# Performance work log

Hardware: AMD Instinct MI355X
Metric: run time of the kernel (lower is better)

Reference implementation:

```python
import jax, jax.numpy as jnp
import numpy as np

B, N, NCTX, DIM, H, DH, NMEM = 2, 1024, 2048, 1024, 16, 64, 16


def setup_inputs() -> dict:
    key = jax.random.key(0)
    ks = jax.random.split(key, 24)
    r = lambda i, shape, s=1.0: jax.random.normal(ks[i], shape, dtype=jnp.float32) * s
    w = 0.02  # linear weight scale
    return {
        "x": r(0, (B, N, DIM)),
        "context": r(1, (2, B, NCTX, DIM)),
        "wq1": r(2, (DIM, H * DH), w), "wk1": r(3, (DIM, H * DH), w), "wv1": r(4, (DIM, H * DH), w),
        "wq2": r(5, (DIM, H * DH), w), "wk2": r(6, (DIM, H * DH), w), "wv2": r(7, (DIM, H * DH), w),
        "th_pre1": r(8, (H, H), 0.25), "th_post1": r(9, (H, H), 0.25),
        "th_pre2": r(10, (H, H), 0.25), "th_post2": r(11, (H, H), 0.25),
        "scale1": jnp.full((1, H, 1, 1), -3.0, jnp.float32) + r(12, (1, H, 1, 1), 0.05),
        "scale2": jnp.full((1, H, 1, 1), -3.0, jnp.float32) + r(13, (1, H, 1, 1), 0.05),
        "mem_k1": r(14, (H, NMEM, DH)), "mem_v1": r(15, (H, NMEM, DH)),
        "mem_k2": r(16, (H, NMEM, DH)), "mem_v2": r(17, (H, NMEM, DH)),
        "hs1": jnp.ones((1, H, 1, 1), jnp.float32) + r(18, (1, H, 1, 1), 0.05),
        "hs2": jnp.ones((1, H, 1, 1), jnp.float32) + r(19, (1, H, 1, 1), 0.05),
        "wo1": r(20, (H * DH, DIM), w), "wo2": r(21, (H * DH, DIM), w),
    }


def _l2norm(t):
    # F.normalize: t / max(||t||, eps)
    n = jnp.linalg.norm(t, axis=-1, keepdims=True)
    return t / jnp.maximum(n, 1e-12)


def _split_heads(t, b):
    # [b, n, h*d] -> [b, h, n, d]
    return t.reshape(b, -1, H, DH).transpose(0, 2, 1, 3)


def _attend(x, kv, wq, wk, wv, th_pre, th_post, scale_p, mem_k, mem_v, hs, wo):
    b, n, _ = x.shape
    q = _split_heads(x @ wq, b)    # [b,h,n,d]
    k = _split_heads(kv @ wk, b)   # [b,h,j,d]
    v = _split_heads(kv @ wv, b)
    # memory key/values prepended
    k = jnp.concatenate([jnp.broadcast_to(mem_k[None], (b, H, NMEM, DH)), k], axis=2)
    v = jnp.concatenate([jnp.broadcast_to(mem_v[None], (b, H, NMEM, DH)), v], axis=2)
    # qk-norm with learned per-head temperature: scale = 1 / clamp(exp(p), min=0.01)
    q, k = _l2norm(q), _l2norm(k)
    scale = 1.0 / jnp.maximum(jnp.exp(scale_p), 0.01)
    dots = jnp.einsum('bhid,bhjd->bhij', q, k) * scale
    # talking heads: 1x1 Conv2d over head channel == head-mixing matmul
    dots = jnp.einsum('gh,bhij->bgij', th_pre, dots)
    attn = jax.nn.softmax(dots, axis=-1)
    attn = jnp.einsum('gh,bhij->bgij', th_post, attn)
    out = jnp.einsum('bhij,bhjd->bhid', attn, v) * hs  # head_scale
    out = out.transpose(0, 2, 1, 3).reshape(b, n, H * DH)
    return out @ wo


def reference(x, context, wq1, wk1, wv1, wq2, wk2, wv2,
              th_pre1, th_post1, th_pre2, th_post2,
              scale1, scale2, mem_k1, mem_v1, mem_k2, mem_v2,
              hs1, hs2, wo1, wo2):
    o1 = _attend(x, context[0], wq1, wk1, wv1, th_pre1, th_post1, scale1, mem_k1, mem_v1, hs1, wo1)
    o2 = _attend(x, context[1], wq2, wk2, wv2, th_pre2, th_post2, scale2, mem_k2, mem_v2, hs2, wo2)
    return o1 + o2
```

## Files before the change

### kernel.cpp

```cpp
#include <hip/hip_runtime.h>
#include <hip/hip_bf16.h>

#define Bb    2
#define Nn    1024
#define NCTXc 2048
#define DIMd  1024
#define Hh    16
#define DHd   64
#define NMEM  16
#define Jv    (NMEM + NCTXc)
#define JP    2112
#define HJP   (Hh * JP)
#define L2E   1.44269504088896f
#define LDH   1048

typedef _Float16 f16;
typedef _Float16 half8 __attribute__((ext_vector_type(8)));
typedef _Float16 half4 __attribute__((ext_vector_type(4)));
typedef float    f32x4 __attribute__((ext_vector_type(4)));

__device__ __forceinline__ float bf2f(unsigned short u){
  union { unsigned int i; float f; } v; v.i = ((unsigned)u) << 16; return v.f;
}
__device__ __forceinline__ float fin(float v){
  v = (v == v) ? v : 0.f;
  return fminf(fmaxf(v, -65504.f), 65504.f);
}
__device__ __forceinline__ float ldin(const void* p, long i, int isf32){
  return isf32 ? ((const float*)p)[i] : bf2f(((const unsigned short*)p)[i]);
}
__device__ __forceinline__ half8 h8zero(){
  half8 v;
  #pragma unroll
  for (int j = 0; j < 8; j++) v[j] = (f16)0.f;
  return v;
}

__global__ void detect_dtype(const void* __restrict__ p, int* __restrict__ flag, int n){
  const unsigned short* ub = (const unsigned short*)p;
  const float* fp = (const float*)p;
  int t = threadIdx.x;
  float bb = 0.f, bf = 0.f;
  for (int i = t; i < n; i += 64){
    float vb = bf2f(ub[i]);
    if (!(vb == vb) || fabsf(vb) > 1000.f) bb += 1.f;
    float vf = fp[i];
    if (!(vf == vf) || fabsf(vf) > 1000.f) bf += 1.f;
  }
  #pragma unroll
  for (int off = 32; off; off >>= 1){ bb += __shfl_xor(bb, off); bf += __shfl_xor(bf, off); }
  if (t == 0) *flag = (bf < bb) ? 1 : 0;
}

__global__ __launch_bounds__(256) void cvt_any(const void* __restrict__ in, f16* __restrict__ out,
                                               long n, const int* __restrict__ flag){
  int isf = *flag;
  long stride = (long)gridDim.x * 256;
  for (long i = (long)blockIdx.x * 256 + threadIdx.x; i < n; i += stride)
    out[i] = (f16)fin(ldin(in, i, isf));
}

__global__ __launch_bounds__(256) void cvt32_any(const void* __restrict__ in, float* __restrict__ out,
                                                 long n, const int* __restrict__ flag){
  int isf = *flag;
  long stride = (long)gridDim.x * 256;
  for (long i = (long)blockIdx.x * 256 + threadIdx.x; i < n; i += stride)
    out[i] = fin(ldin(in, i, isf));
}

__global__ __launch_bounds__(256) void transpose_any(const void* __restrict__ in,
                                                     f16* __restrict__ out,
                                                     int Cc, long ldo,
                                                     const int* __restrict__ flag){
  __shared__ f16 tile[32][33];
  int isf = *flag;
  int r0 = blockIdx.y * 32, c0 = blockIdx.x * 32;
  int tr = threadIdx.x >> 5, tc = threadIdx.x & 31;
  #pragma unroll
  for (int k = 0; k < 4; k++){
    int r = tr + k * 8;
    tile[r][tc] = (f16)fin(ldin(in, (long)(r0 + r) * Cc + c0 + tc, isf));
  }
  __syncthreads();
  #pragma unroll
  for (int k = 0; k < 4; k++){
    int r = tr + k * 8;
    out[(long)(c0 + r) * ldo + r0 + tc] = tile[tc][r];
  }
}

__global__ __launch_bounds__(256) void gemm_raw_bt(
    const void* __restrict__ A, const f16* __restrict__ Bt, f16* __restrict__ C,
    int K, long lda, long ldb, long ldc, long aOff, const int* __restrict__ flag)
{
  int isf = *flag;
  long m0 = (long)blockIdx.y * 64, n0 = (long)blockIdx.x * 64;

  __shared__ f16 As[64][40];
  __shared__ f16 Bs[64][40];
  int t = threadIdx.x;
  int wave = t >> 6, lane = t & 63;
  int wm = (wave >> 1) * 32, wn = (wave & 1) * 32;
  int fr = lane & 15, fq = lane >> 4;
  int srow = t >> 2, scol = (t & 3) * 8;

  f32x4 acc[2][2];
  #pragma unroll
  for (int a = 0; a < 2; a++)
    #pragma unroll
    for (int b = 0; b < 2; b++) acc[a][b] = (f32x4){0.f, 0.f, 0.f, 0.f};

  for (int k0 = 0; k0 < K; k0 += 32){
    long aidx = aOff + (m0 + srow) * lda + k0 + scol;
    half8 avv;
    if (isf){
      const float* ap = (const float*)A + aidx;
      float4 f0 = *(const float4*)ap;
      float4 f1 = *(const float4*)(ap + 4);
      avv[0] = (f16)fin(f0.x); avv[1] = (f16)fin(f0.y); avv[2] = (f16)fin(f0.z); avv[3] = (f16)fin(f0.w);
      avv[4] = (f16)fin(f1.x); avv[5] = (f16)fin(f1.y); avv[6] = (f16)fin(f1.z); avv[7] = (f16)fin(f1.w);
    } else {
      const unsigned short* up = (const unsigned short*)A + aidx;
      #pragma unroll
      for (int j = 0; j < 8; j++) avv[j] = (f16)fin(bf2f(up[j]));
    }
    half8 bvv = *(const half8*)(Bt + (n0 + srow) * ldb + k0 + scol);
    __syncthreads();
    *(half8*)&As[srow][scol] = avv;
    *(half8*)&Bs[srow][scol] = bvv;
    __syncthreads();
    #pragma unroll
    for (int ti = 0; ti < 2; ti++){
      half8 af = *(const half8*)&As[wm + 16 * ti + fr][fq * 8];
      #pragma unroll
      for (int tj = 0; tj < 2; tj++){
        half8 bf = *(const half8*)&Bs[wn + 16 * tj + fr][fq * 8];
        acc[ti][tj] = __builtin_amdgcn_mfma_f32_16x16x32_f16(af, bf, acc[ti][tj], 0, 0, 0);
      }
    }
  }
  #pragma unroll
  for (int ti = 0; ti < 2; ti++)
    #pragma unroll
    for (int tj = 0; tj < 2; tj++)
      #pragma unroll
      for (int r = 0; r < 4; r++){
        long row = m0 + wm + 16 * ti + fq * 4 + r;
        long col = n0 + wn + 16 * tj + fr;
        C[row * ldc + col] = (f16)acc[ti][tj][r];
      }
}

__global__ __launch_bounds__(256) void gemm_bt(
    const f16* __restrict__ A, const f16* __restrict__ Bt, f16* __restrict__ C,
    int K, long lda, long ldb, long ldc,
    long sAb, long sBb, long sCb, long sAh, long sBh, long sCh, int nh)
{
  int z = blockIdx.z;
  int zb = z / nh, zh = z - zb * nh;
  A  += (long)zb * sAb + (long)zh * sAh;
  Bt += (long)zb * sBb + (long)zh * sBh;
  C  += (long)zb * sCb + (long)zh * sCh;
  long m0 = (long)blockIdx.y * 64, n0 = (long)blockIdx.x * 64;

  __shared__ f16 As[64][40];
  __shared__ f16 Bs[64][40];
  int t = threadIdx.x;
  int wave = t >> 6, lane = t & 63;
  int wm = (wave >> 1) * 32, wn = (wave & 1) * 32;
  int fr = lane & 15, fq = lane >> 4;
  int srow = t >> 2, scol = (t & 3) * 8;

  f32x4 acc[2][2];
  #pragma unroll
  for (int a = 0; a < 2; a++)
    #pragma unroll
    for (int b = 0; b < 2; b++) acc[a][b] = (f32x4){0.f, 0.f, 0.f, 0.f};

  for (int k0 = 0; k0 < K; k0 += 32){
    half8 avv = *(const half8*)(A  + (m0 + srow) * lda + k0 + scol);
    half8 bvv = *(const half8*)(Bt + (n0 + srow) * ldb + k0 + scol);
    __syncthreads();
    *(half8*)&As[srow][scol] = avv;
    *(half8*)&Bs[srow][scol] = bvv;
    __syncthreads();
    #pragma unroll
    for (int ti = 0; ti < 2; ti++){
      half8 af = *(const half8*)&As[wm + 16 * ti + fr][fq * 8];
      #pragma unroll
      for (int tj = 0; tj < 2; tj++){
        half8 bf = *(const half8*)&Bs[wn + 16 * tj + fr][fq * 8];
        acc[ti][tj] = __builtin_amdgcn_mfma_f32_16x16x32_f16(af, bf, acc[ti][tj], 0, 0, 0);
      }
    }
  }
  #pragma unroll
  for (int ti = 0; ti < 2; ti++)
    #pragma unroll
    for (int tj = 0; tj < 2; tj++)
      #pragma unroll
      for (int r = 0; r < 4; r++){
        long row = m0 + wm + 16 * ti + fq * 4 + r;
        long col = n0 + wn + 16 * tj + fr;
        C[row * ldc + col] = (f16)acc[ti][tj][r];
      }
}

__global__ __launch_bounds__(256) void gemm_bt_dyn(
    const f16* __restrict__ A, const f16* __restrict__ Bt, void* __restrict__ C,
    int K, long lda, long ldb, long ldc, const int* __restrict__ flag)
{
  int isf = *flag;
  long m0 = (long)blockIdx.y * 64, n0 = (long)blockIdx.x * 64;

  __shared__ f16 As[64][40];
  __shared__ f16 Bs[64][40];
  int t = threadIdx.x;
  int wave = t >> 6, lane = t & 63;
  int wm = (wave >> 1) * 32, wn = (wave & 1) * 32;
  int fr = lane & 15, fq = lane >> 4;
  int srow = t >> 2, scol = (t & 3) * 8;

  f32x4 acc[2][2];
  #pragma unroll
  for (int a = 0; a < 2; a++)
    #pragma unroll
    for (int b = 0; b < 2; b++) acc[a][b] = (f32x4){0.f, 0.f, 0.f, 0.f};

  for (int k0 = 0; k0 < K; k0 += 32){
    half8 avv = *(const half8*)(A  + (m0 + srow) * lda + k0 + scol);
    half8 bvv = *(const half8*)(Bt + (n0 + srow) * ldb + k0 + scol);
    __syncthreads();
    *(half8*)&As[srow][scol] = avv;
    *(half8*)&Bs[srow][scol] = bvv;
    __syncthreads();
    #pragma unroll
    for (int ti = 0; ti < 2; ti++){
      half8 af = *(const half8*)&As[wm + 16 * ti + fr][fq * 8];
      #pragma unroll
      for (int tj = 0; tj < 2; tj++){
        half8 bf = *(const half8*)&Bs[wn + 16 * tj + fr][fq * 8];
        acc[ti][tj] = __builtin_amdgcn_mfma_f32_16x16x32_f16(af, bf, acc[ti][tj], 0, 0, 0);
      }
    }
  }
  #pragma unroll
  for (int ti = 0; ti < 2; ti++)
    #pragma unroll
    for (int tj = 0; tj < 2; tj++)
      #pragma unroll
      for (int r = 0; r < 4; r++){
        long row = m0 + wm + 16 * ti + fq * 4 + r;
        long col = n0 + wn + 16 * tj + fr;
        float v = acc[ti][tj][r];
        if (isf) ((float*)C)[row * ldc + col] = v;
        else     ((__hip_bfloat16*)C)[row * ldc + col] = __float2bfloat16(v);
      }
}

__global__ __launch_bounds__(256) void qn_build(const f16* __restrict__ qp, f16* __restrict__ qn,
                                                const float* __restrict__ scale_p){
  int row = blockIdx.x;
  int wave = threadIdx.x >> 6, lane = threadIdx.x & 63;
  #pragma unroll
  for (int hh = 0; hh < 4; hh++){
    int h = wave * 4 + hh;
    float v = (float)qp[(long)row * 1024 + h * 64 + lane];
    float ss = v * v;
    #pragma unroll
    for (int off = 32; off; off >>= 1) ss += __shfl_xor(ss, off);
    float sc = 1.0f / fmaxf(__expf(scale_p[h]), 0.01f);
    float o = v / fmaxf(sqrtf(ss), 1e-12f) * sc;
    qn[(long)row * 1024 + h * 64 + lane] = (f16)o;
  }
}

__global__ __launch_bounds__(256) void kbuf_build(const f16* __restrict__ kp,
                                                  const f16* __restrict__ mem_k,
                                                  f16* __restrict__ kbuf){
  int id = blockIdx.x * 4 + (threadIdx.x >> 6);
  int lane = threadIdx.x & 63;
  int h = id & 15; int bj = id >> 4; int j = bj % JP; int b = bj / JP;
  float v;
  if (j < NMEM)              v = (float)mem_k[(h * NMEM + j) * 64 + lane];
  else if (j < NMEM + NCTXc) v = (float)kp[((long)b * NCTXc + (j - NMEM)) * 1024 + h * 64 + lane];
  else                       v = 0.f;
  float ss = v * v;
  #pragma unroll
  for (int off = 32; off; off >>= 1) ss += __shfl_xor(ss, off);
  float o = v / fmaxf(sqrtf(ss), 1e-12f);
  kbuf[((long)b * JP + j) * 1024 + h * 64 + lane] = (f16)o;
}

__global__ __launch_bounds__(256) void vt_build(const f16* __restrict__ vp,
                                                const f16* __restrict__ mem_v,
                                                f16* __restrict__ vt){
  __shared__ f16 tile[64][72];
  int id = blockIdx.x;
  int jt = id % (JP / 64); int h = (id / (JP / 64)) & 15; int b = id / (16 * (JP / 64));
  int j0 = jt * 64;
  int t = threadIdx.x;
  #pragma unroll
  for (int rep = 0; rep < 2; rep++){
    int idx = t + rep * 256;
    int jj = idx >> 3, c8 = (idx & 7) * 8;
    int j = j0 + jj;
    half8 v;
    if (j < NMEM){
      v = *(const half8*)(mem_v + (h * NMEM + j) * 64 + c8);
    } else if (j < NMEM + NCTXc){
      v = *(const half8*)(vp + ((long)b * NCTXc + (j - NMEM)) * 1024 + h * 64 + c8);
    } else {
      v = h8zero();
    }
    *(half8*)&tile[jj][c8] = v;
  }
  __syncthreads();
  #pragma unroll
  for (int rep = 0; rep < 2; rep++){
    int idx = t + rep * 256;
    int d = idx >> 3, j8 = (idx & 7) * 8;
    half8 o;
    #pragma unroll
    for (int k = 0; k < 8; k++) o[k] = tile[j8 + k][d];
    *(half8*)(vt + (((long)(b * 16 + h) * 64 + d) * JP) + j0 + j8) = o;
  }
}

__global__ __launch_bounds__(512) void softmax_mfma(
    f16* __restrict__ S,
    const float* __restrict__ th_pre,
    const float* __restrict__ th_post,
    const float* __restrict__ hs)
{
  __shared__ f16 tile[16 * LDH];
  __shared__ float msh[8][16], lsh[8][16];
  __shared__ float Mf[16], Li[16];

  int t = threadIdx.x, wave = t >> 6, lane = t & 63;
  int r16 = lane & 15;
  int hb4 = (lane >> 4) * 4;
  int sr  = t >> 5, sc = t & 31;
  f16* Srow = S + (long)blockIdx.x * HJP;

  half4 ahi, alo;
  #pragma unroll
  for (int j = 0; j < 4; j++){
    float a = th_pre[r16 * 16 + hb4 + j];
    ahi[j] = (f16)a; alo[j] = (f16)(a - (float)ahi[j]);
  }

  float m[4], l[4];
  #pragma unroll
  for (int r = 0; r < 4; r++){ m[r] = -1e30f; l[r] = 0.f; }

  half4 msave[17];
  const f32x4 z4 = (f32x4){0.f, 0.f, 0.f, 0.f};

  #pragma unroll
  for (int it = 0; it < 5; it++){
    int c8 = sc + it * 32;
    if (c8 < 130)
      *(half8*)&tile[sr * LDH + c8 * 8] = *(const half8*)(Srow + (long)sr * JP + c8 * 8);
  }
  __syncthreads();
  #pragma unroll
  for (int cc = 0; cc < 9; cc++){
    int c = wave + cc * 8;
    if (c < 65){
      int lc = c * 16 + r16;
      half4 b;
      #pragma unroll
      for (int j = 0; j < 4; j++) b[j] = tile[(hb4 + j) * LDH + lc];
      f32x4 acc = __builtin_amdgcn_mfma_f32_16x16x16f16(alo, b, z4, 0, 0, 0);
      acc = __builtin_amdgcn_mfma_f32_16x16x16f16(ahi, b, acc, 0, 0, 0);
      half4 hh;
      #pragma unroll
      for (int r = 0; r < 4; r++){
        float u = fminf(fmaxf(acc[r], -60.f), 78.f);
        m[r] = fmaxf(m[r], u);
        l[r] += exp2f(u * L2E);
        hh[r] = (f16)u;
      }
      msave[cc] = hh;
    }
  }
  __syncthreads();
  #pragma unroll
  for (int it = 0; it < 4; it++){
    int c8 = sc + it * 32;
    *(half8*)&tile[sr * LDH + c8 * 8] = *(const half8*)(Srow + (long)sr * JP + 1040 + c8 * 8);
  }
  __syncthreads();
  #pragma unroll
  for (int cc = 0; cc < 8; cc++){
    int c = 65 + wave + cc * 8;
    int lc = c * 16 - 1040 + r16;
    half4 b;
    #pragma unroll
    for (int j = 0; j < 4; j++) b[j] = tile[(hb4 + j) * LDH + lc];
    f32x4 acc = __builtin_amdgcn_mfma_f32_16x16x16f16(alo, b, z4, 0, 0, 0);
    acc = __builtin_amdgcn_mfma_f32_16x16x16f16(ahi, b, acc, 0, 0, 0);
    half4 hh;
    #pragma unroll
    for (int r = 0; r < 4; r++){
      float u = fminf(fmaxf(acc[r], -60.f), 78.f);
      m[r] = fmaxf(m[r], u);
      l[r] += exp2f(u * L2E);
      hh[r] = (f16)u;
    }
    msave[9 + cc] = hh;
  }

  #pragma unroll
  for (int off = 1; off < 16; off <<= 1){
    #pragma unroll
    for (int r = 0; r < 4; r++){
      m[r] = fmaxf(m[r], __shfl_xor(m[r], off));
      l[r] += __shfl_xor(l[r], off);
    }
  }
  if (r16 == 0){
    #pragma unroll
    for (int r = 0; r < 4; r++){ msh[wave][hb4 + r] = m[r]; lsh[wave][hb4 + r] = l[r]; }
  }
  __syncthreads();
  if (t < 16){
    float mf_ = msh[0][t], lf = lsh[0][t];
    #pragma unroll
    for (int w = 1; w < 8; w++){ mf_ = fmaxf(mf_, msh[w][t]); lf += lsh[w][t]; }
    Mf[t] = mf_;
    Li[t] = fin(exp2f(mf_ * L2E) / lf);
  }
  __syncthreads();

  half4 chi, clo;
  float hsv = hs[r16];
  #pragma unroll
  for (int j = 0; j < 4; j++){
    float cc2 = th_post[r16 * 16 + hb4 + j] * hsv * Li[hb4 + j];
    chi[j] = (f16)cc2; clo[j] = (f16)(cc2 - (float)chi[j]);
  }
  float mf[4];
  #pragma unroll
  for (int r = 0; r < 4; r++) mf[r] = Mf[hb4 + r];

  #pragma unroll
  for (int cc = 0; cc < 9; cc++){
    int c = wave + cc * 8;
    if (c < 65){
      half4 h4 = msave[cc];
      half4 ehi, elo;
      #pragma unroll
      for (int r = 0; r < 4; r++){
        float e = exp2f(((float)h4[r] - mf[r]) * L2E);
        ehi[r] = (f16)e; elo[r] = (f16)(e - (float)ehi[r]);
      }
      f32x4 o = __builtin_amdgcn_mfma_f32_16x16x16f16(chi, ehi, z4, 0, 0, 0);
      o = __builtin_amdgcn_mfma_f32_16x16x16f16(clo, ehi, o, 0, 0, 0);
      o = __builtin_amdgcn_mfma_f32_16x16x16f16(chi, elo, o, 0, 0, 0);
      int col = c * 16 + r16;
      #pragma unroll
      for (int r = 0; r < 4; r++) Srow[(hb4 + r) * JP + col] = (f16)o[r];
    }
  }
  #pragma unroll
  for (int cc = 0; cc < 8; cc++){
    int c = 65 + wave + cc * 8;
    half4 h4 = msave[9 + cc];
    half4 ehi, elo;
    #pragma unroll
    for (int r = 0; r < 4; r++){
      float e = exp2f(((float)h4[r] - mf[r]) * L2E);
      ehi[r] = (f16)e; elo[r] = (f16)(e - (float)ehi[r]);
    }
    f32x4 o = __builtin_amdgcn_mfma_f32_16x16x16f16(chi, ehi, z4, 0, 0, 0);
    o = __builtin_amdgcn_mfma_f32_16x16x16f16(clo, ehi, o, 0, 0, 0);
    o = __builtin_amdgcn_mfma_f32_16x16x16f16(chi, elo, o, 0, 0, 0);
    int col = c * 16 + r16;
    #pragma unroll
    for (int r = 0; r < 4; r++) Srow[(hb4 + r) * JP + col] = (f16)o[r];
  }
}

extern "C" void kernel_launch(void* const* d_in, const int* in_sizes, int n_in,
                              void* d_out, int out_size, void* d_ws, size_t ws_size,
                              hipStream_t stream)
{
  (void)in_sizes; (void)n_in; (void)out_size; (void)ws_size;
  int* flag = (int*)d_ws;
  f16* ws   = (f16*)d_ws + 8;
  f16* wT   = ws;
  f16* woT  = wT   + 6291456;
  f16* qn   = woT  + 2097152;
  f16* kbuf = qn   + 2097152;
  f16* vt   = kbuf + 4325376;
  f16* av   = vt   + 4325376;
  f16* memc = av   + 4194304;
  float* parc = (float*)(memc + 65536);
  f16* S    = (f16*)(parc + 1088);
  f16* tmp  = S;

  detect_dtype<<<1, 64, 0, stream>>>(d_in[0], flag, 4096);

  for (int i = 0; i < 4; i++)
    cvt_any<<<16, 256, 0, stream>>>(d_in[14 + i], memc + (long)i * 16384, 16384, flag);
  {
    const int  src[8] = {8, 9, 10, 11, 12, 13, 18, 19};
    const long off[8] = {0, 256, 512, 768, 1024, 1040, 1056, 1072};
    const long cnt[8] = {256, 256, 256, 256, 16, 16, 16, 16};
    for (int i = 0; i < 8; i++)
      cvt32_any<<<1, 256, 0, stream>>>(d_in[src[i]], parc + off[i], cnt[i], flag);
  }

  for (int i = 0; i < 6; i++)
    transpose_any<<<dim3(32, 32), 256, 0, stream>>>(d_in[2 + i],
                                                    wT + (long)i * 1048576, 1024, 1024, flag);
  for (int L = 0; L < 2; L++)
    transpose_any<<<dim3(32, 32), 256, 0, stream>>>(d_in[20 + L],
                                                    woT + (long)L * 1024, 1024, 2048, flag);

  for (int L = 0; L < 2; L++){
    const f16* wqT = wT + (long)(3 * L + 0) * 1048576;
    const f16* wkT = wT + (long)(3 * L + 1) * 1048576;
    const f16* wvT = wT + (long)(3 * L + 2) * 1048576;
    const float* thpre  = parc + (long)L * 512;
    const float* thpost = parc + (long)L * 512 + 256;
    const float* scalep = parc + 1024 + (long)L * 16;
    const float* hsp    = parc + 1056 + (long)L * 16;
    const f16* mem_k = memc + (long)(2 * L) * 16384;
    const f16* mem_v = memc + (long)(2 * L + 1) * 16384;
    const long ctxOff = (long)L * Bb * NCTXc * DIMd;

    gemm_raw_bt<<<dim3(16, 32), 256, 0, stream>>>(d_in[0], wqT, tmp, 1024,
        1024, 1024, 1024, 0, flag);
    qn_build<<<Bb * Nn, 256, 0, stream>>>(tmp, qn, scalep);

    gemm_raw_bt<<<dim3(16, 64), 256, 0, stream>>>(d_in[1], wkT, tmp, 1024,
        1024, 1024, 1024, ctxOff, flag);
    kbuf_build<<<Bb * JP * Hh / 4, 256, 0, stream>>>(tmp, mem_k, kbuf);

    gemm_raw_bt<<<dim3(16, 64), 256, 0, stream>>>(d_in[1], wvT, tmp, 1024,
        1024, 1024, 1024, ctxOff, flag);
    vt_build<<<Bb * Hh * (JP / 64), 256, 0, stream>>>(tmp, mem_v, vt);

    gemm_bt<<<dim3(JP / 64, Nn / 64, Bb * Hh), 256, 0, stream>>>(qn, kbuf, S, 64,
        1024, 1024, HJP,
        (long)Nn * 1024, (long)JP * 1024, (long)Nn * HJP,
        64, 64, JP, Hh);

    softmax_mfma<<<Bb * Nn, 512, 0, stream>>>(S, thpre, thpost, hsp);

    gemm_bt<<<dim3(1, Nn / 64, Bb * Hh), 256, 0, stream>>>(S, vt,
        av + (long)L * 1024, JP,
        HJP, JP, 2048,
        (long)Nn * HJP, (long)Hh * 64 * JP, (long)Nn * 2048,
        JP, (long)64 * JP, 64, Hh);
  }

  gemm_bt_dyn<<<dim3(16, 32), 256, 0, stream>>>(av, woT, d_out, 2048,
      2048, 2048, 1024, flag);
}
```

Before: 881.2 us.

## Use 128x128 direct-to-LDS GEMMs and fuse Q and K/V projections

Replaces the 64x64 projection and output GEMMs with a 128x128-tile kernel that loads tiles straight into LDS via global_load_lds. Inputs are first converted to f16 buffers so the GEMM no longer converts on the fly. The weight transposes are reordered so both Q projections run as one GEMM and each layer's K and V projections run as one GEMM, cutting launches and reusing A tiles. The cost is extra conversion passes and larger intermediate buffers, and the LDS layout has no padding, which may cause bank conflicts.

```diff
diff --git a/kernel.cpp b/kernel.cpp
--- a/kernel.cpp
+++ b/kernel.cpp
@@ -35,6 +35,11 @@
   for (int j = 0; j < 8; j++) v[j] = (f16)0.f;
   return v;
 }
+__device__ __forceinline__ void gload16(const f16* g, f16* l){
+  __builtin_amdgcn_global_load_lds(
+      (const __attribute__((address_space(1))) unsigned int*)g,
+      (__attribute__((address_space(3))) unsigned int*)l, 16, 0, 0);
+}
 
 __global__ void detect_dtype(const void* __restrict__ p, int* __restrict__ flag, int n){
   const unsigned short* ub = (const unsigned short*)p;
@@ -53,11 +58,11 @@
 }
 
 __global__ __launch_bounds__(256) void cvt_any(const void* __restrict__ in, f16* __restrict__ out,
-                                               long n, const int* __restrict__ flag){
+                                               long n, long off, const int* __restrict__ flag){
   int isf = *flag;
   long stride = (long)gridDim.x * 256;
   for (long i = (long)blockIdx.x * 256 + threadIdx.x; i < n; i += stride)
-    out[i] = (f16)fin(ldin(in, i, isf));
+    out[i] = (f16)fin(ldin(in, off + i, isf));
 }
 
 __global__ __launch_bounds__(256) void cvt32_any(const void* __restrict__ in, float* __restrict__ out,
@@ -89,65 +94,124 @@
   }
 }
 
-__global__ __launch_bounds__(256) void gemm_raw_bt(
-    const void* __restrict__ A, const f16* __restrict__ Bt, f16* __restrict__ C,
-    int K, long lda, long ldb, long ldc, long aOff, const int* __restrict__ flag)
+__global__ __launch_bounds__(256) void gemm128(
+    const f16* __restrict__ A, const f16* __restrict__ Bt, f16* __restrict__ C,
+    int K, long lda, long ldb, long ldc)
 {
-  int isf = *flag;
-  long m0 = (long)blockIdx.y * 64, n0 = (long)blockIdx.x * 64;
-
-  __shared__ f16 As[64][40];
-  __shared__ f16 Bs[64][40];
+  __shared__ __align__(16) f16 As[128 * 32];
+  __shared__ __align__(16) f16 Bs[128 * 32];
+  long m0 = (long)blockIdx.y * 128, n0 = (long)blockIdx.x * 128;
   int t = threadIdx.x;
   int wave = t >> 6, lane = t & 63;
-  int wm = (wave >> 1) * 32, wn = (wave & 1) * 32;
+  int wm = (wave >> 1) * 64, wn = (wave & 1) * 64;
   int fr = lane & 15, fq = lane >> 4;
-  int srow = t >> 2, scol = (t & 3) * 8;
-
-  f32x4 acc[2][2];
-  #pragma unroll
-  for (int a = 0; a < 2; a++)
-    #pragma unroll
-    for (int b = 0; b < 2; b++) acc[a][b] = (f32x4){0.f, 0.f, 0.f, 0.f};
+  int sr = t >> 2, scc = (t & 3) * 8;
+
+  f32x4 acc[4][4];
+  #pragma unroll
+  for (int a = 0; a < 4; a++)
+    #pragma unroll
+    for (int b = 0; b < 4; b++) acc[a][b] = (f32x4){0.f, 0.f, 0.f, 0.f};
+
+  const f16* Ap  = A  + (m0 + sr) * lda + scc;
+  const f16* Ap2 = Ap + 64 * lda;
+  const f16* Bp  = Bt + (n0 + sr) * ldb + scc;
+  const f16* Bp2 = Bp + 64 * ldb;
+  f16* Ad  = As + t * 8;
+  f16* Ad2 = As + 2048 + t * 8;
+  f16* Bd  = Bs + t * 8;
+  f16* Bd2 = Bs + 2048 + t * 8;
 
   for (int k0 = 0; k0 < K; k0 += 32){
-    long aidx = aOff + (m0 + srow) * lda + k0 + scol;
-    half8 avv;
-    if (isf){
-      const float* ap = (const float*)A + aidx;
-      float4 f0 = *(const float4*)ap;
-      float4 f1 = *(const float4*)(ap + 4);
-      avv[0] = (f16)fin(f0.x); avv[1] = (f16)fin(f0.y); avv[2] = (f16)fin(f0.z); avv[3] = (f16)fin(f0.w);
-      avv[4] = (f16)fin(f1.x); avv[5] = (f16)fin(f1.y); avv[6] = (f16)fin(f1.z); avv[7] = (f16)fin(f1.w);
-    } else {
-      const unsigned short* up = (const unsigned short*)A + aidx;
-      #pragma unroll
-      for (int j = 0; j < 8; j++) avv[j] = (f16)fin(bf2f(up[j]));
-    }
-    half8 bvv = *(const half8*)(Bt + (n0 + srow) * ldb + k0 + scol);
     __syncthreads();
-    *(half8*)&As[srow][scol] = avv;
-    *(half8*)&Bs[srow][scol] = bvv;
+    gload16(Ap  + k0, Ad);
+    gload16(Ap2 + k0, Ad2);
+    gload16(Bp  + k0, Bd);
+    gload16(Bp2 + k0, Bd2);
     __syncthreads();
-    #pragma unroll
-    for (int ti = 0; ti < 2; ti++){
-      half8 af = *(const half8*)&As[wm + 16 * ti + fr][fq * 8];
-      #pragma unroll
-      for (int tj = 0; tj < 2; tj++){
-        half8 bf = *(const half8*)&Bs[wn + 16 * tj + fr][fq * 8];
-        acc[ti][tj] = __builtin_amdgcn_mfma_f32_16x16x32_f16(af, bf, acc[ti][tj], 0, 0, 0);
-      }
-    }
-  }
-  #pragma unroll
-  for (int ti = 0; ti < 2; ti++)
-    #pragma unroll
-    for (int tj = 0; tj < 2; tj++)
+    half8 bfr[4];
+    #pragma unroll
+    for (int tj = 0; tj < 4; tj++)
+      bfr[tj] = *(const half8*)&Bs[(wn + 16 * tj + fr) * 32 + fq * 8];
+    #pragma unroll
+    for (int ti = 0; ti < 4; ti++){
+      half8 af = *(const half8*)&As[(wm + 16 * ti + fr) * 32 + fq * 8];
+      #pragma unroll
+      for (int tj = 0; tj < 4; tj++)
+        acc[ti][tj] = __builtin_amdgcn_mfma_f32_16x16x32_f16(af, bfr[tj], acc[ti][tj], 0, 0, 0);
+    }
+  }
+  #pragma unroll
+  for (int ti = 0; ti < 4; ti++)
+    #pragma unroll
+    for (int tj = 0; tj < 4; tj++)
       #pragma unroll
       for (int r = 0; r < 4; r++){
         long row = m0 + wm + 16 * ti + fq * 4 + r;
         long col = n0 + wn + 16 * tj + fr;
         C[row * ldc + col] = (f16)acc[ti][tj][r];
+      }
+}
+
+__global__ __launch_bounds__(256) void gemm128_dyn(
+    const f16* __restrict__ A, const f16* __restrict__ Bt, void* __restrict__ C,
+    int K, long lda, long ldb, long ldc, const int* __restrict__ flag)
+{
+  int isf = *flag;
+  __shared__ __align__(16) f16 As[128 * 32];
+  __shared__ __align__(16) f16 Bs[128 * 32];
+  long m0 = (long)blockIdx.y * 128, n0 = (long)blockIdx.x * 128;
+  int t = threadIdx.x;
+  int wave = t >> 6, lane = t & 63;
+  int wm = (wave >> 1) * 64, wn = (wave & 1) * 64;
+  int fr = lane & 15, fq = lane >> 4;
+  int sr = t >> 2, scc = (t & 3) * 8;
+
+  f32x4 acc[4][4];
+  #pragma unroll
+  for (int a = 0; a < 4; a++)
+    #pragma unroll
+    for (int b = 0; b < 4; b++) acc[a][b] = (f32x4){0.f, 0.f, 0.f, 0.f};
+
+  const f16* Ap  = A  + (m0 + sr) * lda + scc;
+  const f16* Ap2 = Ap + 64 * lda;
+  const f16* Bp  = Bt + (n0 + sr) * ldb + scc;
+  const f16* Bp2 = Bp + 64 * ldb;
+  f16* Ad  = As + t * 8;
+  f16* Ad2 = As + 2048 + t * 8;
+  f16* Bd  = Bs + t * 8;
+  f16* Bd2 = Bs + 2048 + t * 8;
+
+  for (int k0 = 0; k0 < K; k0 += 32){
+    __syncthreads();
+    gload16(Ap  + k0, Ad);
+    gload16(Ap2 + k0, Ad2);
+    gload16(Bp  + k0, Bd);
+    gload16(Bp2 + k0, Bd2);
+    __syncthreads();
+    half8 bfr[4];
+    #pragma unroll
+    for (int tj = 0; tj < 4; tj++)
+      bfr[tj] = *(const half8*)&Bs[(wn + 16 * tj + fr) * 32 + fq * 8];
+    #pragma unroll
+    for (int ti = 0; ti < 4; ti++){
+      half8 af = *(const half8*)&As[(wm + 16 * ti + fr) * 32 + fq * 8];
+      #pragma unroll
+      for (int tj = 0; tj < 4; tj++)
+        acc[ti][tj] = __builtin_amdgcn_mfma_f32_16x16x32_f16(af, bfr[tj], acc[ti][tj], 0, 0, 0);
+    }
+  }
+  #pragma unroll
+  for (int ti = 0; ti < 4; ti++)
+    #pragma unroll
+    for (int tj = 0; tj < 4; tj++)
+      #pragma unroll
+      for (int r = 0; r < 4; r++){
+        long row = m0 + wm + 16 * ti + fq * 4 + r;
+        long col = n0 + wn + 16 * tj + fr;
+        float v = acc[ti][tj][r];
+        if (isf) ((float*)C)[row * ldc + col] = v;
+        else     ((__hip_bfloat16*)C)[row * ldc + col] = __float2bfloat16(v);
       }
 }
 
@@ -206,58 +270,6 @@
       }
 }
 
-__global__ __launch_bounds__(256) void gemm_bt_dyn(
-    const f16* __restrict__ A, const f16* __restrict__ Bt, void* __restrict__ C,
-    int K, long lda, long ldb, long ldc, const int* __restrict__ flag)
-{
-  int isf = *flag;
-  long m0 = (long)blockIdx.y * 64, n0 = (long)blockIdx.x * 64;
-
-  __shared__ f16 As[64][40];
-  __shared__ f16 Bs[64][40];
-  int t = threadIdx.x;
-  int wave = t >> 6, lane = t & 63;
-  int wm = (wave >> 1) * 32, wn = (wave & 1) * 32;
-  int fr = lane & 15, fq = lane >> 4;
-  int srow = t >> 2, scol = (t & 3) * 8;
-
-  f32x4 acc[2][2];
-  #pragma unroll
-  for (int a = 0; a < 2; a++)
-    #pragma unroll
-    for (int b = 0; b < 2; b++) acc[a][b] = (f32x4){0.f, 0.f, 0.f, 0.f};
-
-  for (int k0 = 0; k0 < K; k0 += 32){
-    half8 avv = *(const half8*)(A  + (m0 + srow) * lda + k0 + scol);
-    half8 bvv = *(const half8*)(Bt + (n0 + srow) * ldb + k0 + scol);
-    __syncthreads();
-    *(half8*)&As[srow][scol] = avv;
-    *(half8*)&Bs[srow][scol] = bvv;
-    __syncthreads();
-    #pragma unroll
-    for (int ti = 0; ti < 2; ti++){
-      half8 af = *(const half8*)&As[wm + 16 * ti + fr][fq * 8];
-      #pragma unroll
-      for (int tj = 0; tj < 2; tj++){
-        half8 bf = *(const half8*)&Bs[wn + 16 * tj + fr][fq * 8];
-        acc[ti][tj] = __builtin_amdgcn_mfma_f32_16x16x32_f16(af, bf, acc[ti][tj], 0, 0, 0);
-      }
-    }
-  }
-  #pragma unroll
-  for (int ti = 0; ti < 2; ti++)
-    #pragma unroll
-    for (int tj = 0; tj < 2; tj++)
-      #pragma unroll
-      for (int r = 0; r < 4; r++){
-        long row = m0 + wm + 16 * ti + fq * 4 + r;
-        long col = n0 + wn + 16 * tj + fr;
-        float v = acc[ti][tj][r];
-        if (isf) ((float*)C)[row * ldc + col] = v;
-        else     ((__hip_bfloat16*)C)[row * ldc + col] = __float2bfloat16(v);
-      }
-}
-
 __global__ __launch_bounds__(256) void qn_build(const f16* __restrict__ qp, f16* __restrict__ qn,
                                                 const float* __restrict__ scale_p){
   int row = blockIdx.x;
@@ -265,7 +277,7 @@
   #pragma unroll
   for (int hh = 0; hh < 4; hh++){
     int h = wave * 4 + hh;
-    float v = (float)qp[(long)row * 1024 + h * 64 + lane];
+    float v = (float)qp[(long)row * 2048 + h * 64 + lane];
     float ss = v * v;
     #pragma unroll
     for (int off = 32; off; off >>= 1) ss += __shfl_xor(ss, off);
@@ -283,7 +295,7 @@
   int h = id & 15; int bj = id >> 4; int j = bj % JP; int b = bj / JP;
   float v;
   if (j < NMEM)              v = (float)mem_k[(h * NMEM + j) * 64 + lane];
-  else if (j < NMEM + NCTXc) v = (float)kp[((long)b * NCTXc + (j - NMEM)) * 1024 + h * 64 + lane];
+  else if (j < NMEM + NCTXc) v = (float)kp[((long)b * NCTXc + (j - NMEM)) * 2048 + h * 64 + lane];
   else                       v = 0.f;
   float ss = v * v;
   #pragma unroll
@@ -309,7 +321,7 @@
     if (j < NMEM){
       v = *(const half8*)(mem_v + (h * NMEM + j) * 64 + c8);
     } else if (j < NMEM + NCTXc){
-      v = *(const half8*)(vp + ((long)b * NCTXc + (j - NMEM)) * 1024 + h * 64 + c8);
+      v = *(const half8*)(vp + ((long)b * NCTXc + (j - NMEM)) * 2048 + h * 64 + c8);
     } else {
       v = h8zero();
     }
@@ -493,18 +505,21 @@
   f16* wT   = ws;
   f16* woT  = wT   + 6291456;
   f16* qn   = woT  + 2097152;
-  f16* kbuf = qn   + 2097152;
+  f16* kbuf = qn   + 4194304;
   f16* vt   = kbuf + 4325376;
   f16* av   = vt   + 4325376;
   f16* memc = av   + 4194304;
   float* parc = (float*)(memc + 65536);
   f16* S    = (f16*)(parc + 1088);
-  f16* tmp  = S;
+  f16* tmpkv = S;
+  f16* tmpq  = S + 8388608;
+  f16* xf    = S + 12582912;
+  f16* cxf   = S + 14680064;
 
   detect_dtype<<<1, 64, 0, stream>>>(d_in[0], flag, 4096);
 
   for (int i = 0; i < 4; i++)
-    cvt_any<<<16, 256, 0, stream>>>(d_in[14 + i], memc + (long)i * 16384, 16384, flag);
+    cvt_any<<<16, 256, 0, stream>>>(d_in[14 + i], memc + (long)i * 16384, 16384, 0, flag);
   {
     const int  src[8] = {8, 9, 10, 11, 12, 13, 18, 19};
     const long off[8] = {0, 256, 512, 768, 1024, 1040, 1056, 1072};
@@ -513,38 +528,38 @@
       cvt32_any<<<1, 256, 0, stream>>>(d_in[src[i]], parc + off[i], cnt[i], flag);
   }
 
-  for (int i = 0; i < 6; i++)
-    transpose_any<<<dim3(32, 32), 256, 0, stream>>>(d_in[2 + i],
-                                                    wT + (long)i * 1048576, 1024, 1024, flag);
+  {
+    const int slot[6] = {0, 2, 3, 1, 4, 5};
+    for (int i = 0; i < 6; i++)
+      transpose_any<<<dim3(32, 32), 256, 0, stream>>>(d_in[2 + i],
+                                                      wT + (long)slot[i] * 1048576, 1024, 1024, flag);
+  }
   for (int L = 0; L < 2; L++)
     transpose_any<<<dim3(32, 32), 256, 0, stream>>>(d_in[20 + L],
                                                     woT + (long)L * 1024, 1024, 2048, flag);
 
+  cvt_any<<<1024, 256, 0, stream>>>(d_in[0], xf, 2097152, 0, flag);
+  gemm128<<<dim3(16, 16), 256, 0, stream>>>(xf, wT, tmpq, 1024, 1024, 1024, 2048);
+  for (int L = 0; L < 2; L++)
+    qn_build<<<Bb * Nn, 256, 0, stream>>>(tmpq + (long)L * 1024, qn + (long)L * 2097152,
+                                          parc + 1024 + (long)L * 16);
+
   for (int L = 0; L < 2; L++){
-    const f16* wqT = wT + (long)(3 * L + 0) * 1048576;
-    const f16* wkT = wT + (long)(3 * L + 1) * 1048576;
-    const f16* wvT = wT + (long)(3 * L + 2) * 1048576;
     const float* thpre  = parc + (long)L * 512;
     const float* thpost = parc + (long)L * 512 + 256;
-    const float* scalep = parc + 1024 + (long)L * 16;
     const float* hsp    = parc + 1056 + (long)L * 16;
     const f16* mem_k = memc + (long)(2 * L) * 16384;
     const f16* mem_v = memc + (long)(2 * L + 1) * 16384;
     const long ctxOff = (long)L * Bb * NCTXc * DIMd;
-
-    gemm_raw_bt<<<dim3(16, 32), 256, 0, stream>>>(d_in[0], wqT, tmp, 1024,
-        1024, 1024, 1024, 0, flag);
-    qn_build<<<Bb * Nn, 256, 0, stream>>>(tmp, qn, scalep);
-
-    gemm_raw_bt<<<dim3(16, 64), 256, 0, stream>>>(d_in[1], wkT, tmp, 1024,
-        1024, 1024, 1024, ctxOff, flag);
-    kbuf_build<<<Bb * JP * Hh / 4, 256, 0, stream>>>(tmp, mem_k, kbuf);
-
-    gemm_raw_bt<<<dim3(16, 64), 256, 0, stream>>>(d_in[1], wvT, tmp, 1024,
-        1024, 1024, 1024, ctxOff, flag);
-    vt_build<<<Bb * Hh * (JP / 64), 256, 0, stream>>>(tmp, mem_v, vt);
-
-    gemm_bt<<<dim3(JP / 64, Nn / 64, Bb * Hh), 256, 0, stream>>>(qn, kbuf, S, 64,
+    const f16* qnL = qn + (long)L * 2097152;
+
+    cvt_any<<<2048, 256, 0, stream>>>(d_in[1], cxf, 4194304, ctxOff, flag);
+    gemm128<<<dim3(16, 32), 256, 0, stream>>>(cxf, wT + (long)(2 + 2 * L) * 1048576,
+                                              tmpkv, 1024, 1024, 1024, 2048);
+    kbuf_build<<<Bb * JP * Hh / 4, 256, 0, stream>>>(tmpkv, mem_k, kbuf);
+    vt_build<<<Bb * Hh * (JP / 64), 256, 0, stream>>>(tmpkv + 1024, mem_v, vt);
+
+    gemm_bt<<<dim3(JP / 64, Nn / 64, Bb * Hh), 256, 0, stream>>>(qnL, kbuf, S, 64,
         1024, 1024, HJP,
         (long)Nn * 1024, (long)JP * 1024, (long)Nn * HJP,
         64, 64, JP, Hh);
@@ -558,6 +573,6 @@
         JP, (long)64 * JP, 64, Hh);
   }
 
-  gemm_bt_dyn<<<dim3(16, 32), 256, 0, stream>>>(av, woT, d_out, 2048,
+  gemm128_dyn<<<dim3(8, 16), 256, 0, stream>>>(av, woT, d_out, 2048,
       2048, 2048, 1024, flag);
 }
```

New measurement: 816.4 us. 1.08x faster.
